# Optimization experiments

Measured on AMD Instinct MI355X. Metric: run time of the kernel, lower is better.

Reference implementation:

```python
import jax, jax.numpy as jnp
import numpy as np

EPS = 1e-6
BASE_LR = 0.01
MAX_GRAD_NORM = 1.0
CHUNK = 32


def _rms(x, w):
    return x * jax.lax.rsqrt(jnp.mean(x * x, axis=-1, keepdims=True) + EPS) * w


def _mem_fwd(p, x):
    # Memory MLP: linear -> silu -> linear -> RMSNorm -> residual. x: [D]
    h = jax.nn.silu(p['W1'] @ x)
    o = p['W2'] @ h
    return x + _rms(o, p['ln'])


def _loss(p, k, v, w):
    pred = _mem_fwd(p, k)
    return jnp.mean((v - pred) ** 2 * w)


def _binop(a, b):
    # Mamba-like: (a_j*a_i, kv_j + a_j*kv_i)  == torch.addcmul(kv_j, a_j, kv_i)
    (ai, ki), (aj, kj) = a, b
    return (aj * ai, kj + aj * ki)


def _scan_update(past_s, past_m, g, eta, alpha):
    # past_s/past_m: [B,*shape]; g: [B,C,*shape]; eta/alpha: [B,C]
    ext = (1,) * (g.ndim - 2)
    eta_b = eta.reshape(eta.shape + ext)
    alpha_b = alpha.reshape(alpha.shape + ext)
    ones = jnp.ones_like(eta_b[:, :1])
    a = jnp.concatenate([ones, eta_b], axis=1)
    kv = jnp.concatenate([past_s[:, None], -g], axis=1)
    _, s = jax.lax.associative_scan(_binop, (a, kv), axis=1)  # S_t = eta_t*S_{t-1} - g_t
    beta = jnp.concatenate([ones, 1.0 - alpha_b], axis=1)
    mem = jnp.concatenate([past_m[:, None], s[:, 1:]], axis=1)
    _, m = jax.lax.associative_scan(_binop, (beta, mem), axis=1)  # M_t = beta_t*M_{t-1} + S_t
    return s[:, -1], m[:, -1]


def _forward(x, wq, wk, wv, q_norm_w, k_norm_w, alpha_w, theta_w, eta_w, mem_w1, mem_w2, mem_ln):
    B, S, D = x.shape
    NC = S // CHUNK
    params = {'W1': jnp.broadcast_to(mem_w1, (B,) + mem_w1.shape),
              'W2': jnp.broadcast_to(mem_w2, (B,) + mem_w2.shape),
              'ln': jnp.broadcast_to(mem_ln, (B,) + mem_ln.shape)}
    surpr = jax.tree.map(jnp.zeros_like, params)
    xc_all = x.reshape(B, NC, CHUNK, D).transpose(1, 0, 2, 3)  # [NC,B,C,D]
    # per-sample, per-token grad of the TTT loss w.r.t. memory params
    grad_fn = jax.vmap(jax.vmap(jax.grad(_loss), in_axes=(None, 0, 0, 0)),
                       in_axes=(0, 0, 0, 0))

    def step(carry, xc):
        params, surpr = carry
        k = _rms(jax.nn.silu(xc @ wk.T), k_norm_w)      # [B,C,D]
        v = jax.nn.silu(xc @ wv.T)                       # [B,C,D]
        theta = BASE_LR * jax.nn.sigmoid(xc @ theta_w.T)  # [B,C,1] adaptive lr as loss weight
        alpha = jax.nn.sigmoid(xc @ alpha_w.T)[..., 0]     # [B,C] forget gate
        eta = jax.nn.sigmoid(xc @ eta_w.T)[..., 0]         # [B,C] momentum decay
        g = grad_fn(params, k, v, theta)                  # leaves [B,C,*shape]
        # global grad-norm clip per (b, t)
        sq = sum(jnp.sum(gi * gi, axis=tuple(range(2, gi.ndim)))
                 for gi in jax.tree.leaves(g))
        coef = jnp.minimum(MAX_GRAD_NORM / (jnp.sqrt(sq) + 1e-6), 1.0)
        g = jax.tree.map(lambda gi: gi * coef.reshape(coef.shape + (1,) * (gi.ndim - 2)), g)
        new_s, new_p = {}, {}
        for n in params:
            s_n, m_n = _scan_update(surpr[n], params[n], g[n], eta, alpha)
            new_s[n], new_p[n] = s_n, m_n
        return (new_p, new_s), None

    (params, surpr), _ = jax.lax.scan(step, (params, surpr), xc_all)
    # retrieve from the final memory weights
    q = _rms(jax.nn.silu(x @ wq.T), q_norm_w)
    h = jax.nn.silu(jnp.einsum('bsd,bid->bsi', q, params['W1']))
    o = jnp.einsum('bsi,bdi->bsd', h, params['W2'])
    out = q + _rms(o, params['ln'][:, None, :])
    return out


def setup_inputs() -> dict:
    key = jax.random.key(0)
    ks = jax.random.split(key, 12)
    B, S, D, I = 4, 512, 512, 1024

    def xavier(k, shape):
        fan = shape[-1] + shape[-2] if len(shape) > 1 else 2 * shape[-1]
        return jax.random.uniform(k, shape, jnp.float32, -1.0, 1.0) * jnp.sqrt(6.0 / fan)

    return {
        'x': jax.random.normal(ks[0], (B, S, D), jnp.float32),
        'wq': xavier(ks[1], (D, D)),
        'wk': xavier(ks[2], (D, D)),
        'wv': xavier(ks[3], (D, D)),
        'q_norm_w': jnp.ones((D,), jnp.float32),
        'k_norm_w': jnp.ones((D,), jnp.float32),
        'alpha_w': xavier(ks[4], (1, D)),
        'theta_w': xavier(ks[5], (1, D)),
        'eta_w': xavier(ks[6], (1, D)),
        'mem_w1': xavier(ks[7], (I, D)),
        'mem_w2': xavier(ks[8], (D, I)),
        'mem_ln': jnp.ones((D,), jnp.float32),
    }


def reference(x, wq, wk, wv, q_norm_w, k_norm_w, alpha_w, theta_w, eta_w, mem_w1, mem_w2, mem_ln):
    return _forward(x, wq, wk, wv, q_norm_w, k_norm_w, alpha_w, theta_w, eta_w,
                    mem_w1, mem_w2, mem_ln)
```

## Files before the change

kernel.cpp:

```cpp
#include <hip/hip_runtime.h>
#include <hip/hip_bf16.h>

#define B_ 4
#define S_ 512
#define D_ 512
#define I_ 1024
#define C_ 32
#define NC_ 16

#define KBUF (B_*S_*D_)
#define STSZ (B_*I_*D_)
#define HSZ  (B_*I_*C_)
#define DOSZ (B_*C_*D_)
#define OFF_K    0
#define OFF_V    (OFF_K + KBUF)
#define OFF_Q    (OFF_V + KBUF)
#define OFF_TH   (OFF_Q + KBUF)
#define OFF_AL   (OFF_TH + B_*S_)
#define OFF_ET   (OFF_AL + B_*S_)
#define OFF_KN2  (OFF_ET + B_*S_)
#define OFF_SLN  (OFF_KN2 + B_*S_)
#define OFF_MLN  (OFF_SLN + B_*D_)
#define OFF_H2   (OFF_MLN + B_*D_)
#define OFF_Z1   (OFF_H2 + 2*HSZ)
#define OFF_DHP  (OFF_Z1 + HSZ)
#define OFF_DO   (OFF_DHP + HSZ)
#define OFF_DLN  (OFF_DO + DOSZ)
#define OFF_OB   (OFF_DLN + DOSZ)
#define OFF_SLAB (OFF_OB + DOSZ)
#define SLABSTR  256
#define OFF_TICK (OFF_SLAB + NC_*B_*SLABSTR)
#define OFF_FLAG (OFF_TICK + 64)
#define OFF_ORET (OFF_FLAG + 16)
#define OFF_BST  (OFF_ORET + KBUF)
#define OFF_KBFf (OFF_BST + 2*STSZ)
#define OFF_KBTf (OFF_KBFf + KBUF/2)
#define OFF_HIT  (OFF_KBTf + KBUF/2)
#define OFF_HTI  (OFF_HIT + HSZ)
#define OFF_DOB  (OFF_HTI + HSZ)
#define OFF_DOT  (OFF_DOB + DOSZ/2)
#define OFF_HQ   OFF_K

typedef __attribute__((ext_vector_type(8))) short s8v;
typedef __attribute__((ext_vector_type(4))) float f4v;

__device__ __forceinline__ float bf2f(__hip_bfloat16 v){ return __bfloat162float(v); }
__device__ __forceinline__ float bfu2f(unsigned short u){ return __uint_as_float(((unsigned)u)<<16); }
__device__ __forceinline__ unsigned short f2bfu(float f){
  unsigned x = __float_as_uint(f);
  return (unsigned short)((x + 0x7FFFu + ((x>>16)&1u)) >> 16);
}
__device__ __forceinline__ float4 u42f4(ushort4 u){
  float4 r; r.x=bfu2f(u.x); r.y=bfu2f(u.y); r.z=bfu2f(u.z); r.w=bfu2f(u.w); return r;
}
__device__ __forceinline__ ushort4 f42u4(float4 v){
  ushort4 r; r.x=f2bfu(v.x); r.y=f2bfu(v.y); r.z=f2bfu(v.z); r.w=f2bfu(v.w); return r;
}
__device__ __forceinline__ float ldin(const void* p, size_t i, int f){
  return f ? ((const float*)p)[i] : bf2f(((const __hip_bfloat16*)p)[i]);
}
__device__ __forceinline__ float4 ld4g(const void* p, size_t i, int f){
  if(f) return ((const float4*)p)[i>>2];
  return u42f4(((const ushort4*)p)[i>>2]);
}
__device__ __forceinline__ void unp8(uint4 u, float* f){
  f[0]=bfu2f((unsigned short)(u.x&0xffffu)); f[1]=bfu2f((unsigned short)(u.x>>16));
  f[2]=bfu2f((unsigned short)(u.y&0xffffu)); f[3]=bfu2f((unsigned short)(u.y>>16));
  f[4]=bfu2f((unsigned short)(u.z&0xffffu)); f[5]=bfu2f((unsigned short)(u.z>>16));
  f[6]=bfu2f((unsigned short)(u.w&0xffffu)); f[7]=bfu2f((unsigned short)(u.w>>16));
}
__device__ __forceinline__ uint4 pck8(const float* f){
  uint4 u;
  u.x = (unsigned)f2bfu(f[0]) | ((unsigned)f2bfu(f[1])<<16);
  u.y = (unsigned)f2bfu(f[2]) | ((unsigned)f2bfu(f[3])<<16);
  u.z = (unsigned)f2bfu(f[4]) | ((unsigned)f2bfu(f[5])<<16);
  u.w = (unsigned)f2bfu(f[6]) | ((unsigned)f2bfu(f[7])<<16);
  return u;
}

__device__ __forceinline__ float blockReduceSum(float v, float* sm){
  #pragma unroll
  for(int o=32;o>0;o>>=1) v += __shfl_down(v,o,64);
  int wid = threadIdx.x>>6, lane = threadIdx.x&63;
  __syncthreads();
  if(lane==0) sm[wid]=v;
  __syncthreads();
  return sm[0]+sm[1]+sm[2]+sm[3];
}

__global__ void d0_detect(const void* __restrict__ x, float* __restrict__ ws){
  __shared__ int cnt;
  if(threadIdx.x==0) cnt=0;
  __syncthreads();
  unsigned w = ((const unsigned*)x)[(size_t)threadIdx.x*931 + 17];
  int e = (w>>7)&0xFF;
  if(e>=110 && e<=140) atomicAdd(&cnt,1);
  __syncthreads();
  if(threadIdx.x==0) ((int*)(ws+OFF_FLAG))[0] = (cnt<32) ? 1 : 0;
}

__global__ void p0_init(float* __restrict__ ws, const void* __restrict__ w1,
                        const void* __restrict__ w2, const void* __restrict__ ln){
  int f = ((const int*)(ws+OFF_FLAG))[0];
  unsigned short* bst = (unsigned short*)(ws + OFF_BST);
  size_t id = (size_t)blockIdx.x*blockDim.x + threadIdx.x;
  size_t stride = (size_t)gridDim.x*blockDim.x;
  ushort4 z4 = {0,0,0,0};
  for(size_t t4=id; t4<(size_t)(STSZ/4); t4+=stride){
    size_t e4 = t4 % (size_t)(I_*D_/4);
    *(ushort4*)(bst + (size_t)STSZ + t4*4)   = f42u4(ld4g(w1, e4*4, f));
    *(ushort4*)(bst + (size_t)3*STSZ + t4*4) = f42u4(ld4g(w2, e4*4, f));
    *(ushort4*)(bst + t4*4) = z4;
    *(ushort4*)(bst + (size_t)2*STSZ + t4*4) = z4;
  }
  for(size_t t=id; t<(size_t)(B_*D_); t+=stride){
    ws[OFF_MLN+t] = ldin(ln,t % D_,f);
    ws[OFF_SLN+t] = 0.f;
  }
  for(size_t t=id; t<(size_t)(NC_*B_*SLABSTR); t+=stride) ws[OFF_SLAB+t]=0.f;
  int* tick = (int*)(ws + OFF_TICK);
  for(size_t t=id; t<64; t+=stride) tick[t]=0;
}

__global__ void __launch_bounds__(256) p1a(const void* __restrict__ x,
                    const void* __restrict__ wk,
                    const void* __restrict__ wv,
                    const void* __restrict__ wq,
                    float* __restrict__ ws){
  int f = ((const int*)(ws+OFF_FLAG))[0];
  int pid = blockIdx.z;
  const void* W = (pid==0)?wk:((pid==1)?wv:wq);
  float* outp = ws + ((pid==0)?OFF_K:((pid==1)?OFF_V:OFF_Q));
  int r0 = blockIdx.x*64, j0 = blockIdx.y*64;
  __shared__ __align__(16) float xa[32][68], wa[32][68];
  float acc[4][4]={};
  int tx = threadIdx.x & 15, ty = threadIdx.x >> 4;
  for(int k0=0;k0<512;k0+=32){
    #pragma unroll
    for(int q=0;q<2;q++){
      int f4id = threadIdx.x + 256*q;
      int row = f4id>>3, kq = f4id&7;
      float4 v = ld4g(x, (size_t)(r0+row)*512 + k0 + kq*4, f);
      xa[kq*4+0][row]=v.x; xa[kq*4+1][row]=v.y; xa[kq*4+2][row]=v.z; xa[kq*4+3][row]=v.w;
      float4 w = ld4g(W, (size_t)(j0+row)*512 + k0 + kq*4, f);
      wa[kq*4+0][row]=w.x; wa[kq*4+1][row]=w.y; wa[kq*4+2][row]=w.z; wa[kq*4+3][row]=w.w;
    }
    __syncthreads();
    #pragma unroll
    for(int kk=0;kk<32;kk++){
      float4 a4 = *(float4*)&xa[kk][ty*4];
      float4 b4 = *(float4*)&wa[kk][tx*4];
      float a_[4]={a4.x,a4.y,a4.z,a4.w}, b_[4]={b4.x,b4.y,b4.z,b4.w};
      #pragma unroll
      for(int i=0;i<4;i++)
        #pragma unroll
        for(int j=0;j<4;j++) acc[i][j] += a_[i]*b_[j];
    }
    __syncthreads();
  }
  #pragma unroll
  for(int i=0;i<4;i++){
    float4 o4;
    float z0=acc[i][0], z1=acc[i][1], z2=acc[i][2], z3=acc[i][3];
    o4.x = z0/(1.f+expf(-z0)); o4.y = z1/(1.f+expf(-z1));
    o4.z = z2/(1.f+expf(-z2)); o4.w = z3/(1.f+expf(-z3));
    *(float4*)(outp + (size_t)(r0+ty*4+i)*512 + j0 + tx*4) = o4;
  }
}

__global__ void __launch_bounds__(256) p1b(const void* __restrict__ x,
                    const void* __restrict__ kn,
                    const void* __restrict__ qn,
                    const void* __restrict__ aw,
                    const void* __restrict__ tw,
                    const void* __restrict__ ew,
                    float* __restrict__ ws){
  int f = ((const int*)(ws+OFF_FLAG))[0];
  int tok = blockIdx.x; int tid = threadIdx.x;
  __shared__ float sm[8];
  float* krow = ws + OFF_K + (size_t)tok*512;
  float* qrow = ws + OFF_Q + (size_t)tok*512;
  float a = krow[tid], b = krow[tid+256];
  float ss = blockReduceSum(a*a+b*b, sm);
  float n = rsqrtf(ss*(1.f/512.f) + 1e-6f);
  float k1v = a*n*ldin(kn,tid,f);
  float k2v = b*n*ldin(kn,tid+256,f);
  krow[tid]=k1v; krow[tid+256]=k2v;
  float kn2 = blockReduceSum(k1v*k1v+k2v*k2v, sm);
  if(tid==0) ws[OFF_KN2+tok]=kn2;
  a = qrow[tid]; b = qrow[tid+256];
  ss = blockReduceSum(a*a+b*b, sm);
  n = rsqrtf(ss*(1.f/512.f)+1e-6f);
  qrow[tid]=a*n*ldin(qn,tid,f);
  qrow[tid+256]=b*n*ldin(qn,tid+256,f);
  float x1=ldin(x,(size_t)tok*512+tid,f), x2=ldin(x,(size_t)tok*512+tid+256,f);
  float td = blockReduceSum(x1*ldin(tw,tid,f) + x2*ldin(tw,tid+256,f), sm);
  float ad = blockReduceSum(x1*ldin(aw,tid,f) + x2*ldin(aw,tid+256,f), sm);
  float ed = blockReduceSum(x1*ldin(ew,tid,f) + x2*ldin(ew,tid+256,f), sm);
  if(tid==0){
    ws[OFF_TH+tok] = 0.01f/(1.f+expf(-td));
    ws[OFF_AL+tok] = 1.f/(1.f+expf(-ad));
    ws[OFF_ET+tok] = 1.f/(1.f+expf(-ed));
  }
}

__global__ void __launch_bounds__(256) tr_k(float* __restrict__ ws){
  unsigned short* kbf = (unsigned short*)(ws + OFF_KBFf);
  unsigned short* kbt = (unsigned short*)(ws + OFF_KBTf);
  int b = blockIdx.z, st = blockIdx.y, dt = blockIdx.x;
  int s0 = st*64, d0 = dt*64;
  __shared__ unsigned short t[64][72];
  int tid = threadIdx.x;
  #pragma unroll
  for(int q=0;q<4;q++){
    int idx = tid + q*256; int r = idx>>4, cq = idx&15;
    float4 v = *(const float4*)(ws + OFF_K + ((size_t)(b*512 + s0 + r))*512 + d0 + cq*4);
    ushort4 u; u.x=f2bfu(v.x); u.y=f2bfu(v.y); u.z=f2bfu(v.z); u.w=f2bfu(v.w);
    *(ushort4*)&t[r][cq*4] = u;
    *(ushort4*)(kbf + ((size_t)(b*512 + s0 + r))*512 + d0 + cq*4) = u;
  }
  __syncthreads();
  #pragma unroll
  for(int q=0;q<4;q++){
    int idx = tid + q*256; int d = idx>>4, sq = idx&15;
    ushort4 u; u.x=t[sq*4+0][d]; u.y=t[sq*4+1][d]; u.z=t[sq*4+2][d]; u.w=t[sq*4+3][d];
    *(ushort4*)(kbt + ((size_t)(b*512 + d0 + d))*512 + s0 + sq*4) = u;
  }
}

__global__ void __launch_bounds__(256) k1_w1(float* __restrict__ ws, int c){
  unsigned short* bsw1 = (unsigned short*)(ws + OFF_BST);
  unsigned short* bmw1 = bsw1 + STSZ;
  const unsigned short* kbf = (const unsigned short*)(ws + OFF_KBFf);
  const unsigned short* kbt = (const unsigned short*)(ws + OFF_KBTf);
  int b = blockIdx.y, bx = blockIdx.x, tid = threadIdx.x;
  __shared__ float sE[32], sC[32], scal[3];
  if(c>0){
    const float* slab = ws + OFF_SLAB + ((long)(c-1)*B_ + b)*SLABSTR;
    if(tid<32){ sE[tid]=slab[128+tid]; sC[tid]=slab[160+tid]; }
    if(tid>=32 && tid<35) scal[tid-32]=slab[192+(tid-32)];
  }
  __syncthreads();
  float PE = c>0? scal[0]:1.f, PB = c>0? scal[1]:1.f, Q = c>0? scal[2]:0.f;
  if(bx==64){
    if(c>0){
      for(int d=tid; d<512; d+=256){
        float gE=0,gC=0;
        for(int u=0;u<32;u++){
          float dl = ws[OFF_DLN + ((size_t)(b*32+u))*512 + d];
          gE += sE[u]*dl; gC += sC[u]*dl;
        }
        size_t ix = OFF_SLN + (size_t)b*512 + d;
        float sv=ws[ix], mv=ws[ix + (OFF_MLN-OFF_SLN)];
        ws[ix] = PE*sv - gE;
        ws[ix + (OFF_MLN-OFF_SLN)] = PB*mv + Q*sv - gC;
      }
    }
    return;
  }
  __shared__ __align__(16) float gbf[4][2][16][36];
  __shared__ __align__(16) unsigned short ztile[4][16][40];
  __shared__ __align__(16) float zred[4][16][32];
  __shared__ float hredL[32];
  int w = tid>>6, lane = tid&63;
  int i0 = bx*16;
  int col = lane&15, lg = lane>>4;
  int rr = lane>>2, c0 = (lane&3)*8;
  s8v aE = {}, aC = {};
  if(c>0){
    const float* dp = ws + OFF_DHP + ((size_t)(b*I_ + i0 + col))*32 + lg*8;
    float4 dv0 = *(const float4*)dp;
    float4 dv1 = *(const float4*)(dp+4);
    float dv[8] = {dv0.x,dv0.y,dv0.z,dv0.w,dv1.x,dv1.y,dv1.z,dv1.w};
    #pragma unroll
    for(int j=0;j<8;j++){
      aE[j] = (short)f2bfu(sE[lg*8+j]*dv[j]);
      aC[j] = (short)f2bfu(sC[lg*8+j]*dv[j]);
    }
  }
  f4v zacc0 = {0.f,0.f,0.f,0.f}, zacc1 = {0.f,0.f,0.f,0.f};
  const int d0w = w*128;
  const size_t srowbase = ((size_t)(b*I_ + i0))*512;
  const size_t kprow = (size_t)(c-1)*32;
  for(int sl=0; sl<4; sl++){
    int dbase = d0w + sl*32;
    size_t gaddr = srowbase + (size_t)rr*512 + dbase + c0;
    if(c>0){
      #pragma unroll
      for(int t2=0;t2<2;t2++){
        int dt = dbase + t2*16;
        const unsigned short* kp = kbt + ((size_t)(b*512 + dt + col))*512 + kprow + lg*8;
        s8v kB = __builtin_bit_cast(s8v, *(const uint4*)kp);
        f4v zero4 = {0.f,0.f,0.f,0.f};
        f4v gE4 = __builtin_amdgcn_mfma_f32_16x16x32_bf16(aE, kB, zero4, 0,0,0);
        f4v gC4 = __builtin_amdgcn_mfma_f32_16x16x32_bf16(aC, kB, zero4, 0,0,0);
        #pragma unroll
        for(int j=0;j<4;j++){
          gbf[w][0][lg*4+j][t2*16+col] = gE4[j];
          gbf[w][1][lg*4+j][t2*16+col] = gC4[j];
        }
      }
      uint4 su = *(uint4*)(bsw1 + gaddr);
      uint4 mu = *(uint4*)(bmw1 + gaddr);
      float s8[8], m8[8];
      unp8(su, s8); unp8(mu, m8);
      float ns[8], nmv[8];
      #pragma unroll
      for(int j=0;j<8;j++){
        float ge = gbf[w][0][rr][c0+j];
        float gc = gbf[w][1][rr][c0+j];
        ns[j]  = PE*s8[j] - ge;
        nmv[j] = PB*m8[j] + Q*s8[j] - gc;
      }
      *(uint4*)(bsw1 + gaddr) = pck8(ns);
      uint4 nmu = pck8(nmv);
      *(uint4*)(bmw1 + gaddr) = nmu;
      *(uint4*)&ztile[w][rr][c0] = nmu;
    } else {
      uint4 mu = *(uint4*)(bmw1 + gaddr);
      *(uint4*)&ztile[w][rr][c0] = mu;
    }
    if(c<16){
      s8v mA = __builtin_bit_cast(s8v, *(const uint4*)&ztile[w][col][lg*8]);
      const unsigned short* kc0 = kbf + ((size_t)(b*512 + c*32 + col))*512 + dbase + lg*8;
      s8v kB0 = __builtin_bit_cast(s8v, *(const uint4*)kc0);
      s8v kB1 = __builtin_bit_cast(s8v, *(const uint4*)(kc0 + (size_t)16*512));
      zacc0 = __builtin_amdgcn_mfma_f32_16x16x32_bf16(mA, kB0, zacc0, 0,0,0);
      zacc1 = __builtin_amdgcn_mfma_f32_16x16x32_bf16(mA, kB1, zacc1, 0,0,0);
    }
  }
  if(c<16){
    #pragma unroll
    for(int j=0;j<4;j++){
      zred[w][lg*4+j][col]    = zacc0[j];
      zred[w][lg*4+j][16+col] = zacc1[j];
    }
    if(tid<32) hredL[tid]=0.f;
    __syncthreads();
    unsigned short* hit = (unsigned short*)(ws + OFF_HIT) + (size_t)(c&1)*HSZ;
    unsigned short* hti = (unsigned short*)(ws + OFF_HTI) + (size_t)(c&1)*HSZ;
    #pragma unroll
    for(int e=0;e<2;e++){
      int idx = tid*2+e; int row = idx>>5, t = idx&31;
      float z = zred[0][row][t]+zred[1][row][t]+zred[2][row][t]+zred[3][row][t];
      size_t zb = ((size_t)(b*I_ + i0 + row))*32 + t;
      ws[OFF_Z1+zb] = z;
      float h = z/(1.f+expf(-z));
      unsigned short hb = f2bfu(h);
      hit[zb] = hb;
      hti[((size_t)(b*C_+t))*I_ + i0 + row] = hb;
      atomicAdd(&hredL[t], h*h);
    }
    __syncthreads();
    if(tid<32) atomicAdd(ws + OFF_SLAB + ((size_t)c*B_ + b)*SLABSTR + tid, hredL[tid]);
  }
}

__global__ void __launch_bounds__(256) k2_w2(float* __restrict__ ws, int c){
  unsigned short* bsw2 = (unsigned short*)(ws + OFF_BST) + (size_t)2*STSZ;
  unsigned short* bmw2 = bsw2 + STSZ;
  const unsigned short* hitp = (const unsigned short*)(ws + OFF_HIT) + (size_t)((c-1)&1)*HSZ;
  const unsigned short* htic = (const unsigned short*)(ws + OFF_HTI) + (size_t)(c&1)*HSZ;
  const unsigned short* dotb = (const unsigned short*)(ws + OFF_DOT);
  int b = blockIdx.y, bx = blockIdx.x, tid = threadIdx.x;
  int d0 = bx*16;
  __shared__ float sE[32], sC[32], scal[3];
  __shared__ __align__(16) float gbf[4][2][16][36];
  __shared__ __align__(16) unsigned short ztile[4][16][40];
  __shared__ __align__(16) float ored[4][16][32];
  if(c>0){
    const float* slab = ws + OFF_SLAB + ((long)(c-1)*B_+b)*SLABSTR;
    if(tid<32){ sE[tid]=slab[128+tid]; sC[tid]=slab[160+tid]; }
    if(tid>=32&&tid<35) scal[tid-32]=slab[192+tid-32];
  }
  __syncthreads();
  float PE = c>0?scal[0]:1.f, PB=c>0?scal[1]:1.f, Q=c>0?scal[2]:0.f;
  int w = tid>>6, lane = tid&63;
  int col = lane&15, lg = lane>>4;
  int rr = lane>>2, c0 = (lane&3)*8;
  s8v aE = {}, aC = {};
  if(c>0){
    const unsigned short* dp = dotb + ((size_t)(b*D_ + d0 + col))*32 + lg*8;
    float dv[8]; unp8(*(const uint4*)dp, dv);
    #pragma unroll
    for(int j=0;j<8;j++){
      aE[j] = (short)f2bfu(sE[lg*8+j]*dv[j]);
      aC[j] = (short)f2bfu(sC[lg*8+j]*dv[j]);
    }
  }
  f4v oacc0 = {0.f,0.f,0.f,0.f}, oacc1 = {0.f,0.f,0.f,0.f};
  const size_t srowbase = ((size_t)(b*D_ + d0))*1024;
  size_t ga0 = srowbase + (size_t)rr*1024 + w*256 + c0;
  uint4 su={0,0,0,0}, mu, svn=su, mvn;
  if(c>0) su = *(uint4*)(bsw2 + ga0);
  mu = *(uint4*)(bmw2 + ga0);
  for(int sl=0; sl<8; sl++){
    int ibase = w*256 + sl*32;
    size_t gaddr = srowbase + (size_t)rr*1024 + ibase + c0;
    if(sl<7){
      if(c>0) svn = *(uint4*)(bsw2 + gaddr + 32);
      mvn = *(uint4*)(bmw2 + gaddr + 32);
    }
    if(c>0){
      #pragma unroll
      for(int t2=0;t2<2;t2++){
        const unsigned short* hp = hitp + ((size_t)(b*I_ + ibase + t2*16 + col))*32 + lg*8;
        s8v hB = __builtin_bit_cast(s8v, *(const uint4*)hp);
        f4v zero4 = {0.f,0.f,0.f,0.f};
        f4v gE4 = __builtin_amdgcn_mfma_f32_16x16x32_bf16(aE, hB, zero4, 0,0,0);
        f4v gC4 = __builtin_amdgcn_mfma_f32_16x16x32_bf16(aC, hB, zero4, 0,0,0);
        #pragma unroll
        for(int j=0;j<4;j++){
          gbf[w][0][lg*4+j][t2*16+col] = gE4[j];
          gbf[w][1][lg*4+j][t2*16+col] = gC4[j];
        }
      }
      float s8[8], m8[8];
      unp8(su, s8); unp8(mu, m8);
      float ns[8], nmv[8];
      #pragma unroll
      for(int j=0;j<8;j++){
        ns[j]  = PE*s8[j] - gbf[w][0][rr][c0+j];
        nmv[j] = PB*m8[j] + Q*s8[j] - gbf[w][1][rr][c0+j];
      }
      *(uint4*)(bsw2 + gaddr) = pck8(ns);
      uint4 nmu = pck8(nmv);
      *(uint4*)(bmw2 + gaddr) = nmu;
      *(uint4*)&ztile[w][rr][c0] = nmu;
    } else {
      *(uint4*)&ztile[w][rr][c0] = mu;
    }
    if(c<16){
      s8v mA = __builtin_bit_cast(s8v, *(const uint4*)&ztile[w][col][lg*8]);
      const unsigned short* hb = htic + ((size_t)(b*C_+col))*I_ + ibase + lg*8;
      s8v hB0 = __builtin_bit_cast(s8v, *(const uint4*)hb);
      s8v hB1 = __builtin_bit_cast(s8v, *(const uint4*)(hb + (size_t)16*I_));
      oacc0 = __builtin_amdgcn_mfma_f32_16x16x32_bf16(mA, hB0, oacc0, 0,0,0);
      oacc1 = __builtin_amdgcn_mfma_f32_16x16x32_bf16(mA, hB1, oacc1, 0,0,0);
    }
    su = svn; mu = mvn;
  }
  if(c<16){
    #pragma unroll
    for(int j=0;j<4;j++){
      ored[w][lg*4+j][col]    = oacc0[j];
      ored[w][lg*4+j][16+col] = oacc1[j];
    }
    __syncthreads();
    #pragma unroll
    for(int e=0;e<2;e++){
      int idx = tid*2+e; int row = idx>>5, t = idx&31;
      float o = ored[0][row][t]+ored[1][row][t]+ored[2][row][t]+ored[3][row][t];
      ws[OFF_OB + ((size_t)(b*C_+t))*512 + d0 + row] = o;
    }
  }
}

__global__ void __launch_bounds__(256) k3_rms(float* __restrict__ ws, int c){
  int t = blockIdx.x, b = blockIdx.y, tid=threadIdx.x;
  __shared__ float sm[8];
  int tok = b*S_ + c*32 + t;
  const float* orow = ws + OFF_OB + ((size_t)(b*32+t))*512;
  const float* krow = ws + OFF_K + (size_t)tok*512;
  const float* vrow = ws + OFF_V + (size_t)tok*512;
  const float* lrow = ws + OFF_MLN + (size_t)b*512;
  float th = ws[OFF_TH + tok];
  float o1=orow[tid], o2=orow[tid+256];
  float mu = blockReduceSum(o1*o1+o2*o2, sm)*(1.f/512.f);
  float n = rsqrtf(mu + 1e-6f);
  float l1=lrow[tid], l2=lrow[tid+256];
  float k1=krow[tid], k2=krow[tid+256];
  float v1=vrow[tid], v2=vrow[tid+256];
  float c2 = 2.f*th*(1.f/512.f);
  float u1 = c2*(k1 + o1*n*l1 - v1);
  float u2 = c2*(k2 + o2*n*l2 - v2);
  float s1 = blockReduceSum(u1*l1*o1 + u2*l2*o2, sm);
  float dln1 = u1*o1*n, dln2v = u2*o2*n;
  float f = n*n*n*s1*(1.f/512.f);
  float do1 = n*l1*u1 - f*o1;
  float do2 = n*l2*u2 - f*o2;
  float don2 = blockReduceSum(do1*do1+do2*do2, sm);
  float dl2s = blockReduceSum(dln1*dln1+dln2v*dln2v, sm);
  float* dorow = ws + OFF_DO + ((size_t)(b*32+t))*512;
  float* dlrow = ws + OFF_DLN + ((size_t)(b*32+t))*512;
  dorow[tid]=do1; dorow[tid+256]=do2;
  dlrow[tid]=dln1; dlrow[tid+256]=dln2v;
  unsigned short* dob = (unsigned short*)(ws + OFF_DOB);
  unsigned short* dotb = (unsigned short*)(ws + OFF_DOT);
  dob[((size_t)(b*C_+t))*512 + tid]       = f2bfu(do1);
  dob[((size_t)(b*C_+t))*512 + tid + 256] = f2bfu(do2);
  dotb[((size_t)(b*D_ + tid))*32 + t]       = f2bfu(do1);
  dotb[((size_t)(b*D_ + tid + 256))*32 + t] = f2bfu(do2);
  if(tid==0){
    float* slab = ws + OFF_SLAB + ((size_t)c*B_+b)*SLABSTR;
    slab[64+t]=don2; slab[96+t]=dl2s;
  }
}

__global__ void __launch_bounds__(256) k4_dh(float* __restrict__ ws, int c){
  unsigned short* bmw2 = (unsigned short*)(ws + OFF_BST) + (size_t)3*STSZ;
  const unsigned short* dob = (const unsigned short*)(ws + OFF_DOB);
  int bx = blockIdx.x, b = blockIdx.y, tid = threadIdx.x;
  int i0 = bx*16;
  __shared__ unsigned short m2u[16][520];
  __shared__ __align__(16) float dred[4][16][32];
  __shared__ float red[32], coefl[32], bsufl[32];
  __shared__ int lastf;
  #pragma unroll
  for(int q=0;q<4;q++){
    int idx = tid + q*256; int d = idx>>1, half = idx&1;
    uint4 v = *(const uint4*)(bmw2 + ((size_t)(b*D_+d))*1024 + i0 + half*8);
    unsigned short tmp[8]; *(uint4*)tmp = v;
    #pragma unroll
    for(int jj=0;jj<8;jj++) m2u[half*8+jj][d] = tmp[jj];
  }
  if(tid<32) red[tid]=0.f;
  __syncthreads();
  int w = tid>>6, lane = tid&63;
  int col = lane&15, lg = lane>>4;
  f4v acc0 = {0.f,0.f,0.f,0.f}, acc1 = {0.f,0.f,0.f,0.f};
  #pragma unroll
  for(int ks=0;ks<4;ks++){
    int k0 = w*128 + ks*32;
    s8v mA = __builtin_bit_cast(s8v, *(const uint4*)&m2u[col][k0 + lg*8]);
    const unsigned short* dp = dob + ((size_t)(b*C_+col))*512 + k0 + lg*8;
    s8v dB0 = __builtin_bit_cast(s8v, *(const uint4*)dp);
    s8v dB1 = __builtin_bit_cast(s8v, *(const uint4*)(dp + (size_t)16*512));
    acc0 = __builtin_amdgcn_mfma_f32_16x16x32_bf16(mA, dB0, acc0, 0,0,0);
    acc1 = __builtin_amdgcn_mfma_f32_16x16x32_bf16(mA, dB1, acc1, 0,0,0);
  }
  #pragma unroll
  for(int j=0;j<4;j++){
    dred[w][lg*4+j][col]    = acc0[j];
    dred[w][lg*4+j][16+col] = acc1[j];
  }
  __syncthreads();
  #pragma unroll
  for(int e=0;e<2;e++){
    int idx = tid*2+e; int row = idx>>5, t = idx&31;
    float dh = dred[0][row][t]+dred[1][row][t]+dred[2][row][t]+dred[3][row][t];
    size_t zb = ((size_t)(b*I_ + i0 + row))*32 + t;
    float z = ws[OFF_Z1+zb];
    float s = 1.f/(1.f+expf(-z));
    float dp_ = dh * s*(1.f + z*(1.f-s));
    ws[OFF_DHP+zb] = dp_;
    atomicAdd(&red[t], dp_*dp_);
  }
  __syncthreads();
  float* slab = ws + OFF_SLAB + ((size_t)c*B_+b)*SLABSTR;
  if(tid<32) atomicAdd(&slab[32+tid], red[tid]);
  __threadfence();
  __syncthreads();
  if(tid==0){
    int* tick = (int*)(ws+OFF_TICK);
    lastf = (atomicAdd(&tick[c*B_+b],1) == 63) ? 1 : 0;
  }
  __syncthreads();
  if(!lastf) return;
  if(tid<32){
    float sqd = atomicAdd(&slab[32+tid], 0.f);
    float hn  = atomicAdd(&slab[0+tid], 0.f);
    float don2 = slab[64+tid], dl2 = slab[96+tid];
    float kn2 = ws[OFF_KN2 + b*S_ + c*32 + tid];
    float sq = sqd*kn2 + don2*hn + dl2;
    coefl[tid] = fminf(1.f/(sqrtf(sq)+1e-6f), 1.f);
  }
  __syncthreads();
  if(tid==0){
    const float* eta = ws + OFF_ET + b*S_ + c*32;
    const float* alp = ws + OFF_AL + b*S_ + c*32;
    float Esuf=1.f, Bsuf=1.f, cu=1.f;
    for(int u=31;u>=0;u--){
      if(u<31){
        float e1 = eta[u+1], b1 = 1.f-alp[u+1];
        Esuf *= e1; Bsuf *= b1;
        cu = Bsuf + e1*cu;
      }
      bsufl[u]=Bsuf;
      slab[128+u] = Esuf*coefl[u];
      slab[160+u] = cu*coefl[u];
    }
    float PE = Esuf*eta[0];
    float PB = Bsuf*(1.f-alp[0]);
    float Q=0.f, Epre=1.f;
    for(int t2=0;t2<32;t2++){ Epre *= eta[t2]; Q += bsufl[t2]*Epre; }
    slab[192]=PE; slab[193]=PB; slab[194]=Q;
  }
}

__global__ void __launch_bounds__(256) r1_gemm(float* __restrict__ ws){
  unsigned short* bmw1 = (unsigned short*)(ws + OFF_BST) + STSZ;
  int b = blockIdx.z;
  int s0 = blockIdx.x*64, i0 = blockIdx.y*64;
  __shared__ __align__(16) float qa[32][68], wa[32][68];
  float acc[4][4]={};
  int tx = threadIdx.x&15, ty = threadIdx.x>>4;
  const float* qb = ws + OFF_Q + (size_t)b*S_*D_;
  const unsigned short* w1b = bmw1 + (size_t)b*I_*D_;
  for(int k0=0;k0<512;k0+=32){
    #pragma unroll
    for(int q=0;q<2;q++){
      int f4id = threadIdx.x + 256*q;
      int row = f4id>>3, kq = f4id&7;
      float4 v = *(const float4*)(qb + (size_t)(s0+row)*512 + k0 + kq*4);
      qa[kq*4+0][row]=v.x; qa[kq*4+1][row]=v.y; qa[kq*4+2][row]=v.z; qa[kq*4+3][row]=v.w;
      float4 w = u42f4(*(const ushort4*)(w1b + (size_t)(i0+row)*512 + k0 + kq*4));
      wa[kq*4+0][row]=w.x; wa[kq*4+1][row]=w.y; wa[kq*4+2][row]=w.z; wa[kq*4+3][row]=w.w;
    }
    __syncthreads();
    #pragma unroll
    for(int kk=0;kk<32;kk++){
      float4 a4 = *(float4*)&qa[kk][ty*4];
      float4 b4 = *(float4*)&wa[kk][tx*4];
      float a_[4]={a4.x,a4.y,a4.z,a4.w}, b_[4]={b4.x,b4.y,b4.z,b4.w};
      #pragma unroll
      for(int i=0;i<4;i++)
        #pragma unroll
        for(int j=0;j<4;j++) acc[i][j]+=a_[i]*b_[j];
    }
    __syncthreads();
  }
  float* hq = ws + OFF_HQ + (size_t)b*S_*I_;
  #pragma unroll
  for(int i=0;i<4;i++){
    float4 o4;
    o4.x = acc[i][0]/(1.f+expf(-acc[i][0])); o4.y = acc[i][1]/(1.f+expf(-acc[i][1]));
    o4.z = acc[i][2]/(1.f+expf(-acc[i][2])); o4.w = acc[i][3]/(1.f+expf(-acc[i][3]));
    *(float4*)(hq + (size_t)(s0+ty*4+i)*1024 + i0 + tx*4) = o4;
  }
}

__global__ void __launch_bounds__(256) r2_gemm(float* __restrict__ ws){
  unsigned short* bmw2 = (unsigned short*)(ws + OFF_BST) + (size_t)3*STSZ;
  int b=blockIdx.z;
  int s0=blockIdx.x*64, d0=blockIdx.y*64;
  __shared__ __align__(16) float ha[32][68], wa[32][68];
  float acc[4][4]={};
  int tx=threadIdx.x&15, ty=threadIdx.x>>4;
  const float* hq = ws + OFF_HQ + (size_t)b*S_*I_;
  const unsigned short* w2b = bmw2 + (size_t)b*D_*I_;
  for(int k0=0;k0<1024;k0+=32){
    #pragma unroll
    for(int q=0;q<2;q++){
      int f4id = threadIdx.x + 256*q;
      int row = f4id>>3, kq = f4id&7;
      float4 v = *(const float4*)(hq + (size_t)(s0+row)*1024 + k0 + kq*4);
      ha[kq*4+0][row]=v.x; ha[kq*4+1][row]=v.y; ha[kq*4+2][row]=v.z; ha[kq*4+3][row]=v.w;
      float4 w = u42f4(*(const ushort4*)(w2b + (size_t)(d0+row)*1024 + k0 + kq*4));
      wa[kq*4+0][row]=w.x; wa[kq*4+1][row]=w.y; wa[kq*4+2][row]=w.z; wa[kq*4+3][row]=w.w;
    }
    __syncthreads();
    #pragma unroll
    for(int kk=0;kk<32;kk++){
      float4 a4 = *(float4*)&ha[kk][ty*4];
      float4 b4 = *(float4*)&wa[kk][tx*4];
      float a_[4]={a4.x,a4.y,a4.z,a4.w}, b_[4]={b4.x,b4.y,b4.z,b4.w};
      #pragma unroll
      for(int i=0;i<4;i++)
        #pragma unroll
        for(int j=0;j<4;j++) acc[i][j]+=a_[i]*b_[j];
    }
    __syncthreads();
  }
  float* od = ws + OFF_ORET + (size_t)b*S_*D_;
  #pragma unroll
  for(int i=0;i<4;i++){
    float4 o4 = {acc[i][0],acc[i][1],acc[i][2],acc[i][3]};
    *(float4*)(od + (size_t)(s0+ty*4+i)*512 + d0 + tx*4) = o4;
  }
}

__global__ void __launch_bounds__(256) r3_out(float* __restrict__ ws, void* __restrict__ out){
  int f = ((const int*)(ws+OFF_FLAG))[0];
  int tok=blockIdx.x, tid=threadIdx.x;
  int b = tok >> 9;
  __shared__ float sm[8];
  const float* orow = ws + OFF_ORET + (size_t)tok*512;
  const float* qrow = ws + OFF_Q + (size_t)tok*512;
  const float* lrow = ws + OFF_MLN + (size_t)b*512;
  float o1=orow[tid], o2=orow[tid+256];
  float mu = blockReduceSum(o1*o1+o2*o2, sm)*(1.f/512.f);
  float n = rsqrtf(mu+1e-6f);
  float r1v = qrow[tid]     + o1*n*lrow[tid];
  float r2v = qrow[tid+256] + o2*n*lrow[tid+256];
  if(f){
    ((float*)out)[(size_t)tok*512+tid]     = r1v;
    ((float*)out)[(size_t)tok*512+tid+256] = r2v;
  } else {
    ((__hip_bfloat16*)out)[(size_t)tok*512+tid]     = __float2bfloat16(r1v);
    ((__hip_bfloat16*)out)[(size_t)tok*512+tid+256] = __float2bfloat16(r2v);
  }
}

extern "C" void kernel_launch(void* const* d_in, const int* in_sizes, int n_in,
                              void* d_out, int out_size, void* d_ws, size_t ws_size,
                              hipStream_t stream) {
  const void* x  = d_in[0];
  const void* wq = d_in[1];
  const void* wk = d_in[2];
  const void* wv = d_in[3];
  const void* qn = d_in[4];
  const void* kn = d_in[5];
  const void* aw = d_in[6];
  const void* tw = d_in[7];
  const void* ew = d_in[8];
  const void* w1 = d_in[9];
  const void* w2 = d_in[10];
  const void* ln = d_in[11];
  float* ws = (float*)d_ws;

  d0_detect<<<1,64,0,stream>>>(x, ws);
  p0_init<<<2048,256,0,stream>>>(ws, w1, w2, ln);
  p1a<<<dim3(32,8,3),256,0,stream>>>(x, wk, wv, wq, ws);
  p1b<<<2048,256,0,stream>>>(x, kn, qn, aw, tw, ew, ws);
  tr_k<<<dim3(8,8,4),256,0,stream>>>(ws);
  for(int c=0;c<=16;c++){
    k1_w1<<<dim3(65,4),256,0,stream>>>(ws, c);
    k2_w2<<<dim3(32,4),256,0,stream>>>(ws, c);
    if(c<16){
      k3_rms<<<dim3(32,4),256,0,stream>>>(ws, c);
      k4_dh<<<dim3(64,4),256,0,stream>>>(ws, c);
    }
  }
  r1_gemm<<<dim3(8,16,4),256,0,stream>>>(ws);
  r2_gemm<<<dim3(8,8,4),256,0,stream>>>(ws);
  r3_out<<<2048,256,0,stream>>>(ws, d_out);
}
```

Measured before the change: 1.119 ms.

## Move projection and readout GEMMs to bf16 MFMA with pre-converted operands

Replaces the fp32 shared-memory SIMT GEMMs in the input projection (p1a) and the readout GEMMs (r1, r2) with bf16 MFMA 16x16x32 instructions that read operands straight from global memory. New conversion kernels cast x, wk/wv/wq and q to bf16 scratch buffers, and the hidden readout activations are stored as bf16. The aim is to cut FP32 ALU time and halve operand traffic. In exchange it adds extra conversion launches and bf16 rounding error, and it reuses workspace regions (ORET, KBFf, V, K) as scratch, which depends on their lifetimes not overlapping.

```diff
diff --git a/kernel.cpp b/kernel.cpp
--- a/kernel.cpp
+++ b/kernel.cpp
@@ -39,7 +39,6 @@
 #define OFF_HTI  (OFF_HIT + HSZ)
 #define OFF_DOB  (OFF_HTI + HSZ)
 #define OFF_DOT  (OFF_DOB + DOSZ/2)
-#define OFF_HQ   OFF_K
 
 typedef __attribute__((ext_vector_type(8))) short s8v;
 typedef __attribute__((ext_vector_type(4))) float f4v;
@@ -122,50 +121,49 @@
   for(size_t t=id; t<64; t+=stride) tick[t]=0;
 }
 
-__global__ void __launch_bounds__(256) p1a(const void* __restrict__ x,
-                    const void* __restrict__ wk,
-                    const void* __restrict__ wv,
-                    const void* __restrict__ wq,
-                    float* __restrict__ ws){
+__global__ void __launch_bounds__(256) cvt_in(const void* __restrict__ x,
+                    const void* __restrict__ wk, const void* __restrict__ wv,
+                    const void* __restrict__ wq, float* __restrict__ ws){
   int f = ((const int*)(ws+OFF_FLAG))[0];
+  unsigned short* xbf = (unsigned short*)(ws + OFF_ORET);
+  unsigned short* wbf = (unsigned short*)(ws + OFF_KBFf);
+  size_t id = (size_t)blockIdx.x*blockDim.x + threadIdx.x;
+  size_t stride = (size_t)gridDim.x*blockDim.x;
+  for(size_t t4=id; t4<(size_t)(KBUF/4); t4+=stride)
+    *(ushort4*)(xbf + t4*4) = f42u4(ld4g(x, t4*4, f));
+  for(size_t t4=id; t4<(size_t)(3*D_*D_/4); t4+=stride){
+    int pid = (int)(t4 / (D_*D_/4));
+    size_t e4 = t4 % (size_t)(D_*D_/4);
+    const void* W = (pid==0)?wk:((pid==1)?wv:wq);
+    *(ushort4*)(wbf + t4*4) = f42u4(ld4g(W, e4*4, f));
+  }
+}
+
+__global__ void __launch_bounds__(256) p1a(float* __restrict__ ws){
+  const unsigned short* xbf = (const unsigned short*)(ws + OFF_ORET);
+  const unsigned short* wbf = (const unsigned short*)(ws + OFF_KBFf);
   int pid = blockIdx.z;
-  const void* W = (pid==0)?wk:((pid==1)?wv:wq);
   float* outp = ws + ((pid==0)?OFF_K:((pid==1)?OFF_V:OFF_Q));
+  const unsigned short* W = wbf + (size_t)pid*D_*D_;
   int r0 = blockIdx.x*64, j0 = blockIdx.y*64;
-  __shared__ __align__(16) float xa[32][68], wa[32][68];
-  float acc[4][4]={};
-  int tx = threadIdx.x & 15, ty = threadIdx.x >> 4;
+  int w = threadIdx.x>>6, lane = threadIdx.x&63;
+  int col = lane&15, lg = lane>>4;
+  f4v acc[4] = {{0,0,0,0},{0,0,0,0},{0,0,0,0},{0,0,0,0}};
   for(int k0=0;k0<512;k0+=32){
-    #pragma unroll
-    for(int q=0;q<2;q++){
-      int f4id = threadIdx.x + 256*q;
-      int row = f4id>>3, kq = f4id&7;
-      float4 v = ld4g(x, (size_t)(r0+row)*512 + k0 + kq*4, f);
-      xa[kq*4+0][row]=v.x; xa[kq*4+1][row]=v.y; xa[kq*4+2][row]=v.z; xa[kq*4+3][row]=v.w;
-      float4 w = ld4g(W, (size_t)(j0+row)*512 + k0 + kq*4, f);
-      wa[kq*4+0][row]=w.x; wa[kq*4+1][row]=w.y; wa[kq*4+2][row]=w.z; wa[kq*4+3][row]=w.w;
-    }
-    __syncthreads();
-    #pragma unroll
-    for(int kk=0;kk<32;kk++){
-      float4 a4 = *(float4*)&xa[kk][ty*4];
-      float4 b4 = *(float4*)&wa[kk][tx*4];
-      float a_[4]={a4.x,a4.y,a4.z,a4.w}, b_[4]={b4.x,b4.y,b4.z,b4.w};
-      #pragma unroll
-      for(int i=0;i<4;i++)
-        #pragma unroll
-        for(int j=0;j<4;j++) acc[i][j] += a_[i]*b_[j];
-    }
-    __syncthreads();
-  }
-  #pragma unroll
-  for(int i=0;i<4;i++){
-    float4 o4;
-    float z0=acc[i][0], z1=acc[i][1], z2=acc[i][2], z3=acc[i][3];
-    o4.x = z0/(1.f+expf(-z0)); o4.y = z1/(1.f+expf(-z1));
-    o4.z = z2/(1.f+expf(-z2)); o4.w = z3/(1.f+expf(-z3));
-    *(float4*)(outp + (size_t)(r0+ty*4+i)*512 + j0 + tx*4) = o4;
-  }
+    s8v bB = __builtin_bit_cast(s8v, *(const uint4*)(W + (size_t)(j0 + w*16 + col)*512 + k0 + lg*8));
+    #pragma unroll
+    for(int rg=0;rg<4;rg++){
+      s8v aA = __builtin_bit_cast(s8v, *(const uint4*)(xbf + (size_t)(r0 + rg*16 + col)*512 + k0 + lg*8));
+      acc[rg] = __builtin_amdgcn_mfma_f32_16x16x32_bf16(aA, bB, acc[rg], 0,0,0);
+    }
+  }
+  #pragma unroll
+  for(int rg=0;rg<4;rg++)
+    #pragma unroll
+    for(int j=0;j<4;j++){
+      float z = acc[rg][j];
+      outp[(size_t)(r0 + rg*16 + lg*4 + j)*512 + j0 + w*16 + col] = z/(1.f+expf(-z));
+    }
 }
 
 __global__ void __launch_bounds__(256) p1b(const void* __restrict__ x,
@@ -588,86 +586,66 @@
   }
 }
 
+__global__ void __launch_bounds__(256) cvt_q(float* __restrict__ ws){
+  unsigned short* qbf = (unsigned short*)(ws + OFF_V);
+  size_t id = (size_t)blockIdx.x*blockDim.x + threadIdx.x;
+  float4 v = *(const float4*)(ws + OFF_Q + id*4);
+  *(ushort4*)(qbf + id*4) = f42u4(v);
+}
+
 __global__ void __launch_bounds__(256) r1_gemm(float* __restrict__ ws){
-  unsigned short* bmw1 = (unsigned short*)(ws + OFF_BST) + STSZ;
+  const unsigned short* qbf = (const unsigned short*)(ws + OFF_V);
+  const unsigned short* bmw1 = (const unsigned short*)(ws + OFF_BST) + STSZ;
+  unsigned short* hqb = (unsigned short*)(ws + OFF_K);
   int b = blockIdx.z;
   int s0 = blockIdx.x*64, i0 = blockIdx.y*64;
-  __shared__ __align__(16) float qa[32][68], wa[32][68];
-  float acc[4][4]={};
-  int tx = threadIdx.x&15, ty = threadIdx.x>>4;
-  const float* qb = ws + OFF_Q + (size_t)b*S_*D_;
+  int w = threadIdx.x>>6, lane = threadIdx.x&63;
+  int col = lane&15, lg = lane>>4;
+  const unsigned short* qb = qbf + (size_t)b*S_*D_;
   const unsigned short* w1b = bmw1 + (size_t)b*I_*D_;
+  f4v acc[4] = {{0,0,0,0},{0,0,0,0},{0,0,0,0},{0,0,0,0}};
   for(int k0=0;k0<512;k0+=32){
-    #pragma unroll
-    for(int q=0;q<2;q++){
-      int f4id = threadIdx.x + 256*q;
-      int row = f4id>>3, kq = f4id&7;
-      float4 v = *(const float4*)(qb + (size_t)(s0+row)*512 + k0 + kq*4);
-      qa[kq*4+0][row]=v.x; qa[kq*4+1][row]=v.y; qa[kq*4+2][row]=v.z; qa[kq*4+3][row]=v.w;
-      float4 w = u42f4(*(const ushort4*)(w1b + (size_t)(i0+row)*512 + k0 + kq*4));
-      wa[kq*4+0][row]=w.x; wa[kq*4+1][row]=w.y; wa[kq*4+2][row]=w.z; wa[kq*4+3][row]=w.w;
-    }
-    __syncthreads();
-    #pragma unroll
-    for(int kk=0;kk<32;kk++){
-      float4 a4 = *(float4*)&qa[kk][ty*4];
-      float4 b4 = *(float4*)&wa[kk][tx*4];
-      float a_[4]={a4.x,a4.y,a4.z,a4.w}, b_[4]={b4.x,b4.y,b4.z,b4.w};
-      #pragma unroll
-      for(int i=0;i<4;i++)
-        #pragma unroll
-        for(int j=0;j<4;j++) acc[i][j]+=a_[i]*b_[j];
-    }
-    __syncthreads();
-  }
-  float* hq = ws + OFF_HQ + (size_t)b*S_*I_;
-  #pragma unroll
-  for(int i=0;i<4;i++){
-    float4 o4;
-    o4.x = acc[i][0]/(1.f+expf(-acc[i][0])); o4.y = acc[i][1]/(1.f+expf(-acc[i][1]));
-    o4.z = acc[i][2]/(1.f+expf(-acc[i][2])); o4.w = acc[i][3]/(1.f+expf(-acc[i][3]));
-    *(float4*)(hq + (size_t)(s0+ty*4+i)*1024 + i0 + tx*4) = o4;
-  }
+    s8v bB = __builtin_bit_cast(s8v, *(const uint4*)(w1b + (size_t)(i0 + w*16 + col)*512 + k0 + lg*8));
+    #pragma unroll
+    for(int rg=0;rg<4;rg++){
+      s8v aA = __builtin_bit_cast(s8v, *(const uint4*)(qb + (size_t)(s0 + rg*16 + col)*512 + k0 + lg*8));
+      acc[rg] = __builtin_amdgcn_mfma_f32_16x16x32_bf16(aA, bB, acc[rg], 0,0,0);
+    }
+  }
+  unsigned short* hb = hqb + (size_t)b*S_*I_;
+  #pragma unroll
+  for(int rg=0;rg<4;rg++)
+    #pragma unroll
+    for(int j=0;j<4;j++){
+      float z = acc[rg][j];
+      hb[(size_t)(s0 + rg*16 + lg*4 + j)*1024 + i0 + w*16 + col] = f2bfu(z/(1.f+expf(-z)));
+    }
 }
 
 __global__ void __launch_bounds__(256) r2_gemm(float* __restrict__ ws){
-  unsigned short* bmw2 = (unsigned short*)(ws + OFF_BST) + (size_t)3*STSZ;
+  const unsigned short* hqb = (const unsigned short*)(ws + OFF_K);
+  const unsigned short* bmw2 = (const unsigned short*)(ws + OFF_BST) + (size_t)3*STSZ;
   int b=blockIdx.z;
   int s0=blockIdx.x*64, d0=blockIdx.y*64;
-  __shared__ __align__(16) float ha[32][68], wa[32][68];
-  float acc[4][4]={};
-  int tx=threadIdx.x&15, ty=threadIdx.x>>4;
-  const float* hq = ws + OFF_HQ + (size_t)b*S_*I_;
+  int w = threadIdx.x>>6, lane = threadIdx.x&63;
+  int col = lane&15, lg = lane>>4;
+  const unsigned short* hb = hqb + (size_t)b*S_*I_;
   const unsigned short* w2b = bmw2 + (size_t)b*D_*I_;
+  f4v acc[4] = {{0,0,0,0},{0,0,0,0},{0,0,0,0},{0,0,0,0}};
   for(int k0=0;k0<1024;k0+=32){
-    #pragma unroll
-    for(int q=0;q<2;q++){
-      int f4id = threadIdx.x + 256*q;
-      int row = f4id>>3, kq = f4id&7;
-      float4 v = *(const float4*)(hq + (size_t)(s0+row)*1024 + k0 + kq*4);
-      ha[kq*4+0][row]=v.x; ha[kq*4+1][row]=v.y; ha[kq*4+2][row]=v.z; ha[kq*4+3][row]=v.w;
-      float4 w = u42f4(*(const ushort4*)(w2b + (size_t)(d0+row)*1024 + k0 + kq*4));
-      wa[kq*4+0][row]=w.x; wa[kq*4+1][row]=w.y; wa[kq*4+2][row]=w.z; wa[kq*4+3][row]=w.w;
-    }
-    __syncthreads();
-    #pragma unroll
-    for(int kk=0;kk<32;kk++){
-      float4 a4 = *(float4*)&ha[kk][ty*4];
-      float4 b4 = *(float4*)&wa[kk][tx*4];
-      float a_[4]={a4.x,a4.y,a4.z,a4.w}, b_[4]={b4.x,b4.y,b4.z,b4.w};
-      #pragma unroll
-      for(int i=0;i<4;i++)
-        #pragma unroll
-        for(int j=0;j<4;j++) acc[i][j]+=a_[i]*b_[j];
-    }
-    __syncthreads();
+    s8v bB = __builtin_bit_cast(s8v, *(const uint4*)(w2b + (size_t)(d0 + w*16 + col)*1024 + k0 + lg*8));
+    #pragma unroll
+    for(int rg=0;rg<4;rg++){
+      s8v aA = __builtin_bit_cast(s8v, *(const uint4*)(hb + (size_t)(s0 + rg*16 + col)*1024 + k0 + lg*8));
+      acc[rg] = __builtin_amdgcn_mfma_f32_16x16x32_bf16(aA, bB, acc[rg], 0,0,0);
+    }
   }
   float* od = ws + OFF_ORET + (size_t)b*S_*D_;
   #pragma unroll
-  for(int i=0;i<4;i++){
-    float4 o4 = {acc[i][0],acc[i][1],acc[i][2],acc[i][3]};
-    *(float4*)(od + (size_t)(s0+ty*4+i)*512 + d0 + tx*4) = o4;
-  }
+  for(int rg=0;rg<4;rg++)
+    #pragma unroll
+    for(int j=0;j<4;j++)
+      od[(size_t)(s0 + rg*16 + lg*4 + j)*512 + d0 + w*16 + col] = acc[rg][j];
 }
 
 __global__ void __launch_bounds__(256) r3_out(float* __restrict__ ws, void* __restrict__ out){
@@ -711,7 +689,8 @@
 
   d0_detect<<<1,64,0,stream>>>(x, ws);
   p0_init<<<2048,256,0,stream>>>(ws, w1, w2, ln);
-  p1a<<<dim3(32,8,3),256,0,stream>>>(x, wk, wv, wq, ws);
+  cvt_in<<<2048,256,0,stream>>>(x, wk, wv, wq, ws);
+  p1a<<<dim3(32,8,3),256,0,stream>>>(ws);
   p1b<<<2048,256,0,stream>>>(x, kn, qn, aw, tw, ew, ws);
   tr_k<<<dim3(8,8,4),256,0,stream>>>(ws);
   for(int c=0;c<=16;c++){
@@ -722,6 +701,7 @@
       k4_dh<<<dim3(64,4),256,0,stream>>>(ws, c);
     }
   }
+  cvt_q<<<1024,256,0,stream>>>(ws);
   r1_gemm<<<dim3(8,16,4),256,0,stream>>>(ws);
   r2_gemm<<<dim3(8,8,4),256,0,stream>>>(ws);
   r3_out<<<2048,256,0,stream>>>(ws, d_out);
```

Result: faster. 1.056 ms (-5.6%).
